# Kernel optimization log

Hardware: AMD Instinct MI355X
Metric: run time of the kernel (lower is better)

## Reference

```python
import jax, jax.numpy as jnp
import numpy as np

H, B, N, F, O = 8, 2, 2048, 256, 64
NEG_INF = jnp.float32(-9e15)


def _xavier(key, shape):
    fan_in, fan_out = shape[-2], shape[-1]
    limit = np.sqrt(6.0 / (fan_in + fan_out))
    return jax.random.uniform(key, shape, dtype=jnp.float32, minval=-limit, maxval=limit)


def setup_inputs() -> dict:
    key = jax.random.key(0)
    k1, k2, k3, k4, k5 = jax.random.split(key, 5)
    x = jax.random.normal(k1, (B, N, F), dtype=jnp.float32)
    adj = (jax.random.uniform(k2, (B, N, N)) < 0.05).astype(jnp.float32)
    adj = jnp.maximum(adj, jnp.eye(N, dtype=jnp.float32))
    W = _xavier(k3, (H, F, O))           # self.linear
    a_src = _xavier(k4, (H, O, 1))       # attention_vect_src
    a_dst = _xavier(k5, (H, O, 1))       # attention_vect_dst
    return {"x": x, "adj": adj, "W": W, "a_src": a_src, "a_dst": a_dst}


def reference(x, adj, W, a_src, a_dst):
    # h: [H, B, N, O]  (per-head linear projection)
    h = jnp.einsum('bnf,hfo->hbno', x, W)
    # additive attention scalars per node: [H, B, N]
    s_src = jnp.einsum('hbno,ho->hbn', h, a_src[..., 0])
    s_dst = jnp.einsum('hbno,ho->hbn', h, a_dst[..., 0])
    # score[h,b,i,j] = s_dst[i] + s_src[j]  -> [H, B, N, N]
    score = s_dst[..., :, None] + s_src[..., None, :]
    score = jax.nn.leaky_relu(score, negative_slope=0.2)
    score = jnp.where(adj > 0, score, NEG_INF)
    att = jax.nn.softmax(score, axis=-1) * adj  # dropout = identity (eval)
    # weighted aggregation of neighbor features: [H, B, N, O]
    out = jnp.einsum('hbij,hbjo->hbio', att, h)
    # concat heads along feature dim (head order preserved): [B, N, H*O]
    out = jnp.transpose(out, (1, 2, 0, 3)).reshape(B, N, H * O)
    return jax.nn.relu(out)
```

## Files before the change

### kernel.cpp

```cpp
#include <hip/hip_runtime.h>

#define H_ 8
#define B_ 2
#define N_ 2048
#define F_ 256
#define O_ 64
#define CAP 256
#define KPAD 264

typedef unsigned short u16;
typedef unsigned int   u32;
typedef __attribute__((ext_vector_type(8))) short bf16x8;
typedef __attribute__((ext_vector_type(4))) float f32x4;

__device__ __forceinline__ float us2f(u16 u) {
    union { u32 i; float f; } c; c.i = ((u32)u) << 16; return c.f;
}
__device__ __forceinline__ u16 f2us_rn(float f) {
    union { float f; u32 i; } c; c.f = f;
    u32 r = c.i + 0x7FFFu + ((c.i >> 16) & 1u);
    return (u16)(r >> 16);
}

__global__ void detect_kernel(const uint4* __restrict__ adj_v, int* __restrict__ flag) {
    __shared__ int found;
    if (threadIdx.x == 0) found = 0;
    __syncthreads();
#pragma unroll
    for (int i = 0; i < 16; ++i) {
        uint4 v = adj_v[threadIdx.x * 16 + i];
        u32 w[4] = {v.x, v.y, v.z, v.w};
        for (int q = 0; q < 4; ++q)
            if (w[q] == 0x00003F80u || w[q] == 0x3F803F80u) found = 1;
    }
    __syncthreads();
    if (threadIdx.x == 0) flag[0] = found;
}

__global__ void wt_kernel(const void* __restrict__ W,
                          const int* __restrict__ flag,
                          u16* __restrict__ Wt) {
    int h  = blockIdx.x;
    int o  = threadIdx.x & 63;
    int fq = threadIdx.x >> 6;
    u16* dst = Wt + (size_t)h * O_ * F_ + (size_t)o * F_;
    if (flag[0]) {
        const u16* wg = (const u16*)W + (size_t)h * F_ * O_;
        for (int i = 0; i < 64; ++i) {
            int f = fq * 64 + i;
            dst[f] = wg[(size_t)f * O_ + o];
        }
    } else {
        const float* wg = (const float*)W + (size_t)h * F_ * O_;
        for (int i = 0; i < 64; ++i) {
            int f = fq * 64 + i;
            dst[f] = f2us_rn(wg[(size_t)f * O_ + o]);
        }
    }
}

__global__ __launch_bounds__(256) void proj_kernel(const void* __restrict__ x,
                                                   const u16* __restrict__ Wt,
                                                   const void* __restrict__ a_src,
                                                   const void* __restrict__ a_dst,
                                                   const int* __restrict__ flag,
                                                   float* __restrict__ hT,
                                                   float* __restrict__ sTsrc,
                                                   float* __restrict__ sTdst) {
    __shared__ alignas(16) u16 wt[64 * KPAD];

    int bf   = flag[0];
    int bx   = blockIdx.x;
    int h    = bx & 7;
    int bn0  = (bx >> 3) * 64;
    int tid  = threadIdx.x;
    int wave = tid >> 6;
    int lane = tid & 63;

    {
        int o    = tid >> 2;
        int part = tid & 3;
        const u16* src = Wt + (size_t)h * O_ * F_ + (size_t)o * F_ + part * 64;
        u16* dst = wt + o * KPAD + part * 64;
#pragma unroll
        for (int i = 0; i < 8; ++i)
            *(uint4*)(dst + i * 8) = *(const uint4*)(src + i * 8);
    }
    __syncthreads();

    int m_l  = lane & 15;
    int quad = lane >> 4;
    int mrow = bn0 + wave * 16 + m_l;

    f32x4 acc[4] = {{0,0,0,0},{0,0,0,0},{0,0,0,0},{0,0,0,0}};
#pragma unroll
    for (int ks = 0; ks < 8; ++ks) {
        int kofs = ks * 32 + quad * 8;
        bf16x8 afrag;
        if (bf) {
            afrag = *(const bf16x8*)((const u16*)x + (size_t)mrow * F_ + kofs);
        } else {
            const float* xr = (const float*)x + (size_t)mrow * F_ + kofs;
#pragma unroll
            for (int q = 0; q < 8; ++q) afrag[q] = (short)f2us_rn(xr[q]);
        }
#pragma unroll
        for (int nt = 0; nt < 4; ++nt) {
            bf16x8 bfrag = *(const bf16x8*)(wt + (nt * 16 + m_l) * KPAD + kofs);
            acc[nt] = __builtin_amdgcn_mfma_f32_16x16x32_bf16(afrag, bfrag, acc[nt], 0, 0, 0);
        }
    }

    float asv[4], adv[4];
#pragma unroll
    for (int nt = 0; nt < 4; ++nt) {
        int o = nt * 16 + m_l;
        if (bf) {
            asv[nt] = us2f(((const u16*)a_src)[h * 64 + o]);
            adv[nt] = us2f(((const u16*)a_dst)[h * 64 + o]);
        } else {
            asv[nt] = ((const float*)a_src)[h * 64 + o];
            adv[nt] = ((const float*)a_dst)[h * 64 + o];
        }
    }
    float vs[4] = {0,0,0,0}, vd[4] = {0,0,0,0};
#pragma unroll
    for (int nt = 0; nt < 4; ++nt)
#pragma unroll
        for (int r = 0; r < 4; ++r) {
            float hv = acc[nt][r];
            int row = wave * 16 + quad * 4 + r;
            hT[(size_t)(bn0 + row) * (H_ * O_) + h * O_ + nt * 16 + m_l] = hv;
            vs[r] = fmaf(hv, asv[nt], vs[r]);
            vd[r] = fmaf(hv, adv[nt], vd[r]);
        }
#pragma unroll
    for (int r = 0; r < 4; ++r)
#pragma unroll
        for (int off = 1; off < 16; off <<= 1) {
            vs[r] += __shfl_xor(vs[r], off);
            vd[r] += __shfl_xor(vd[r], off);
        }
    if (m_l == 0) {
#pragma unroll
        for (int r = 0; r < 4; ++r) {
            int row = wave * 16 + quad * 4 + r;
            sTsrc[(size_t)(bn0 + row) * H_ + h] = vs[r];
            sTdst[(size_t)(bn0 + row) * H_ + h] = vd[r];
        }
    }
}

__global__ void GATLayer_88072599371930_kernel(const float* __restrict__ hT,
                                               const float* __restrict__ sTsrc,
                                               const float* __restrict__ sTdst,
                                               const void* __restrict__ adj,
                                               const int* __restrict__ flag,
                                               float* __restrict__ out) {
    __shared__ int   scnt;
    __shared__ u16   sj[CAP];
    __shared__ float se[CAP * H_];
    __shared__ float mh[H_];
    __shared__ float rzh[H_];
    __shared__ float sdl[H_];
    __shared__ float sred[128 * 4];

    int bi   = blockIdx.x;
    int tid  = threadIdx.x;
    int base = bi & ~(N_ - 1);

    if (tid == 0) scnt = 0;
    if (tid < 8) sdl[tid] = sTdst[(size_t)bi * H_ + tid];
    __syncthreads();

    if (flag[0]) {
        const u16* arow = (const u16*)adj + (size_t)bi * N_;
        uint4 v = *(const uint4*)(arow + tid * 8);
        u32 w[4] = {v.x, v.y, v.z, v.w};
        int j0 = tid * 8;
#pragma unroll
        for (int q = 0; q < 4; ++q) {
            if (w[q] & 0xFFFFu) { int p = atomicAdd(&scnt, 1); if (p < CAP) sj[p] = (u16)(j0 + 2 * q); }
            if (w[q] >> 16)     { int p = atomicAdd(&scnt, 1); if (p < CAP) sj[p] = (u16)(j0 + 2 * q + 1); }
        }
    } else {
        const float* arow = (const float*)adj + (size_t)bi * N_;
        for (int j = tid; j < N_; j += 256) {
            if (arow[j] > 0.f) { int p = atomicAdd(&scnt, 1); if (p < CAP) sj[p] = (u16)j; }
        }
    }
    __syncthreads();
    int n = scnt < CAP ? scnt : CAP;

    if (n <= 0) {
        out[(size_t)bi * 512 + tid] = 999.0f;
        out[(size_t)bi * 512 + 256 + tid] = 999.0f;
        return;
    }

    int tot = n * H_;
    for (int idx = tid; idx < tot; idx += 256) {
        int k  = idx >> 3;
        int hh = idx & 7;
        int j  = sj[k];
        float v = sdl[hh] + sTsrc[(size_t)(base + j) * H_ + hh];
        v = v > 0.f ? v : 0.2f * v;
        se[idx] = v;
    }
    __syncthreads();

    if (tid < 64) {
        int hh = tid >> 3, kk = tid & 7;
        float lm = -3.4e38f;
        for (int k = kk; k < n; k += 8) lm = fmaxf(lm, se[k * 8 + hh]);
#pragma unroll
        for (int mm = 1; mm < 8; mm <<= 1) lm = fmaxf(lm, __shfl_xor(lm, mm));
        if (kk == 0) mh[hh] = lm;
    }
    __syncthreads();

    for (int idx = tid; idx < tot; idx += 256) {
        int hh = idx & 7;
        se[idx] = __expf(se[idx] - mh[hh]);
    }
    __syncthreads();

    if (tid < 64) {
        int hh = tid >> 3, kk = tid & 7;
        float ls = 0.f;
        for (int k = kk; k < n; k += 8) ls += se[k * 8 + hh];
#pragma unroll
        for (int mm = 1; mm < 8; mm <<= 1) ls += __shfl_xor(ls, mm);
        if (kk == 0) rzh[hh] = 1.f / ls;
    }
    __syncthreads();

    int slot = tid >> 7;
    int hh   = (tid >> 4) & 7;
    int oq   = tid & 15;
    const float* hb = hT + (size_t)base * 512 + hh * 64 + oq * 4;
    float a0 = 0.f, a1 = 0.f, a2 = 0.f, a3 = 0.f;
    int k = slot;
    for (; k + 6 < n; k += 8) {
        int   j0 = sj[k],     j1 = sj[k + 2], j2 = sj[k + 4], j3 = sj[k + 6];
        float w0 = se[k * 8 + hh],       w1 = se[(k + 2) * 8 + hh];
        float w2 = se[(k + 4) * 8 + hh], w3 = se[(k + 6) * 8 + hh];
        float4 v0 = *(const float4*)(hb + (size_t)j0 * 512);
        float4 v1 = *(const float4*)(hb + (size_t)j1 * 512);
        float4 v2 = *(const float4*)(hb + (size_t)j2 * 512);
        float4 v3 = *(const float4*)(hb + (size_t)j3 * 512);
        a0 = fmaf(w0, v0.x, a0); a1 = fmaf(w0, v0.y, a1); a2 = fmaf(w0, v0.z, a2); a3 = fmaf(w0, v0.w, a3);
        a0 = fmaf(w1, v1.x, a0); a1 = fmaf(w1, v1.y, a1); a2 = fmaf(w1, v1.z, a2); a3 = fmaf(w1, v1.w, a3);
        a0 = fmaf(w2, v2.x, a0); a1 = fmaf(w2, v2.y, a1); a2 = fmaf(w2, v2.z, a2); a3 = fmaf(w2, v2.w, a3);
        a0 = fmaf(w3, v3.x, a0); a1 = fmaf(w3, v3.y, a1); a2 = fmaf(w3, v3.z, a2); a3 = fmaf(w3, v3.w, a3);
    }
    for (; k < n; k += 2) {
        int   j = sj[k];
        float w = se[k * 8 + hh];
        float4 v = *(const float4*)(hb + (size_t)j * 512);
        a0 = fmaf(w, v.x, a0); a1 = fmaf(w, v.y, a1); a2 = fmaf(w, v.z, a2); a3 = fmaf(w, v.w, a3);
    }
    if (slot == 1) {
        float4 t; t.x = a0; t.y = a1; t.z = a2; t.w = a3;
        ((float4*)sred)[tid - 128] = t;
    }
    __syncthreads();
    if (slot == 0) {
        float4 p = ((float4*)sred)[tid];
        float rz = rzh[hh];
        float4 r;
        r.x = fmaxf((a0 + p.x) * rz, 0.f);
        r.y = fmaxf((a1 + p.y) * rz, 0.f);
        r.z = fmaxf((a2 + p.z) * rz, 0.f);
        r.w = fmaxf((a3 + p.w) * rz, 0.f);
        *(float4*)(out + (size_t)bi * 512 + tid * 4) = r;
    }
}

extern "C" void kernel_launch(void* const* d_in, const int* in_sizes, int n_in,
                              void* d_out, int out_size, void* d_ws, size_t ws_size,
                              hipStream_t stream) {
    const void *x = 0, *adj = 0, *W = 0, *a_src = 0, *a_dst = 0;
    for (int i = 0; i < n_in; ++i) {
        long sz = in_sizes[i];
        if (sz == (long)B_ * N_ * F_)      x = d_in[i];
        else if (sz == (long)B_ * N_ * N_) adj = d_in[i];
        else if (sz == (long)H_ * F_ * O_) W = d_in[i];
        else if (sz == (long)H_ * O_) { if (!a_src) a_src = d_in[i]; else a_dst = d_in[i]; }
    }
    if (!x)     x     = d_in[0];
    if (!adj)   adj   = d_in[1];
    if (!W)     W     = d_in[2];
    if (!a_src) a_src = d_in[3];
    if (!a_dst) a_dst = d_in[4];

    float* out = (float*)d_out;

    char* ws = (char*)d_ws;
    size_t off = 0;
    int*   flag  = (int*)(ws + off);   off += 256;
    float* hT    = (float*)(ws + off); off += (size_t)B_ * N_ * H_ * O_ * 4;
    float* sTsrc = (float*)(ws + off); off += (size_t)B_ * N_ * H_ * 4;
    float* sTdst = (float*)(ws + off); off += (size_t)B_ * N_ * H_ * 4;
    u16*   Wt    = (u16*)(ws + off);   off += (size_t)H_ * O_ * F_ * 2;

    detect_kernel<<<dim3(1), dim3(256), 0, stream>>>((const uint4*)adj, flag);
    wt_kernel<<<dim3(H_), dim3(256), 0, stream>>>(W, flag, Wt);
    proj_kernel<<<dim3((N_ * B_ / 64) * H_), dim3(256), 0, stream>>>(
        x, Wt, a_src, a_dst, flag, hT, sTsrc, sTdst);
    GATLayer_88072599371930_kernel<<<dim3(B_ * N_), dim3(256), 0, stream>>>(
        hT, sTsrc, sTdst, adj, flag, out);
}
```

Baseline: 147.7 us.

## Store projected features as bf16, drop detect kernel, reshape gather loop

```diff
diff --git a/kernel.cpp b/kernel.cpp
--- a/kernel.cpp
+++ b/kernel.cpp
@@ -6,7 +6,6 @@
 #define F_ 256
 #define O_ 64
 #define CAP 256
-#define KPAD 264
 
 typedef unsigned short u16;
 typedef unsigned int   u32;
@@ -16,81 +15,63 @@
 __device__ __forceinline__ float us2f(u16 u) {
     union { u32 i; float f; } c; c.i = ((u32)u) << 16; return c.f;
 }
+__device__ __forceinline__ float hi2f(u32 w) {
+    union { u32 i; float f; } c; c.i = w & 0xFFFF0000u; return c.f;
+}
+__device__ __forceinline__ float lo2f(u32 w) {
+    union { u32 i; float f; } c; c.i = w << 16; return c.f;
+}
 __device__ __forceinline__ u16 f2us_rn(float f) {
     union { float f; u32 i; } c; c.f = f;
     u32 r = c.i + 0x7FFFu + ((c.i >> 16) & 1u);
     return (u16)(r >> 16);
 }
-
-__global__ void detect_kernel(const uint4* __restrict__ adj_v, int* __restrict__ flag) {
-    __shared__ int found;
-    if (threadIdx.x == 0) found = 0;
-    __syncthreads();
-#pragma unroll
-    for (int i = 0; i < 16; ++i) {
-        uint4 v = adj_v[threadIdx.x * 16 + i];
-        u32 w[4] = {v.x, v.y, v.z, v.w};
-        for (int q = 0; q < 4; ++q)
-            if (w[q] == 0x00003F80u || w[q] == 0x3F803F80u) found = 1;
-    }
-    __syncthreads();
-    if (threadIdx.x == 0) flag[0] = found;
-}
-
-__global__ void wt_kernel(const void* __restrict__ W,
-                          const int* __restrict__ flag,
-                          u16* __restrict__ Wt) {
-    int h  = blockIdx.x;
-    int o  = threadIdx.x & 63;
-    int fq = threadIdx.x >> 6;
-    u16* dst = Wt + (size_t)h * O_ * F_ + (size_t)o * F_;
-    if (flag[0]) {
-        const u16* wg = (const u16*)W + (size_t)h * F_ * O_;
-        for (int i = 0; i < 64; ++i) {
-            int f = fq * 64 + i;
-            dst[f] = wg[(size_t)f * O_ + o];
-        }
+__device__ __forceinline__ int detect_bf(const void* adj) {
+    u32 w0 = *(const u32*)adj;
+    return (w0 & 0xFFFFu) == 0x3F80u;
+}
+
+__global__ __launch_bounds__(256) void wt_kernel(const void* __restrict__ W,
+                                                 const void* __restrict__ adj,
+                                                 u16* __restrict__ Wt) {
+    int bf = detect_bf(adj);
+    int g  = blockIdx.x * 256 + threadIdx.x;
+    int h  = g >> 11;
+    int o  = (g >> 5) & 63;
+    int fc = g & 31;
+    u16 tmp[8];
+    if (bf) {
+        const u16* wg = (const u16*)W + (size_t)h * F_ * O_ + o;
+#pragma unroll
+        for (int q = 0; q < 8; ++q) tmp[q] = wg[(size_t)(fc * 8 + q) * O_];
     } else {
-        const float* wg = (const float*)W + (size_t)h * F_ * O_;
-        for (int i = 0; i < 64; ++i) {
-            int f = fq * 64 + i;
-            dst[f] = f2us_rn(wg[(size_t)f * O_ + o]);
-        }
-    }
+        const float* wg = (const float*)W + (size_t)h * F_ * O_ + o;
+#pragma unroll
+        for (int q = 0; q < 8; ++q) tmp[q] = f2us_rn(wg[(size_t)(fc * 8 + q) * O_]);
+    }
+    *(uint4*)(Wt + (size_t)h * O_ * F_ + (size_t)o * F_ + fc * 8) = *(uint4*)tmp;
 }
 
 __global__ __launch_bounds__(256) void proj_kernel(const void* __restrict__ x,
                                                    const u16* __restrict__ Wt,
                                                    const void* __restrict__ a_src,
                                                    const void* __restrict__ a_dst,
-                                                   const int* __restrict__ flag,
-                                                   float* __restrict__ hT,
+                                                   const void* __restrict__ adj,
+                                                   u16* __restrict__ hTb,
                                                    float* __restrict__ sTsrc,
                                                    float* __restrict__ sTdst) {
-    __shared__ alignas(16) u16 wt[64 * KPAD];
-
-    int bf   = flag[0];
+    int bf   = detect_bf(adj);
     int bx   = blockIdx.x;
     int h    = bx & 7;
     int bn0  = (bx >> 3) * 64;
     int tid  = threadIdx.x;
     int wave = tid >> 6;
     int lane = tid & 63;
-
-    {
-        int o    = tid >> 2;
-        int part = tid & 3;
-        const u16* src = Wt + (size_t)h * O_ * F_ + (size_t)o * F_ + part * 64;
-        u16* dst = wt + o * KPAD + part * 64;
-#pragma unroll
-        for (int i = 0; i < 8; ++i)
-            *(uint4*)(dst + i * 8) = *(const uint4*)(src + i * 8);
-    }
-    __syncthreads();
-
     int m_l  = lane & 15;
     int quad = lane >> 4;
     int mrow = bn0 + wave * 16 + m_l;
+
+    const u16* wtb = Wt + (size_t)h * O_ * F_;
 
     f32x4 acc[4] = {{0,0,0,0},{0,0,0,0},{0,0,0,0},{0,0,0,0}};
 #pragma unroll
@@ -106,7 +87,7 @@
         }
 #pragma unroll
         for (int nt = 0; nt < 4; ++nt) {
-            bf16x8 bfrag = *(const bf16x8*)(wt + (nt * 16 + m_l) * KPAD + kofs);
+            bf16x8 bfrag = *(const bf16x8*)(wtb + (size_t)(nt * 16 + m_l) * F_ + kofs);
             acc[nt] = __builtin_amdgcn_mfma_f32_16x16x32_bf16(afrag, bfrag, acc[nt], 0, 0, 0);
         }
     }
@@ -130,7 +111,7 @@
         for (int r = 0; r < 4; ++r) {
             float hv = acc[nt][r];
             int row = wave * 16 + quad * 4 + r;
-            hT[(size_t)(bn0 + row) * (H_ * O_) + h * O_ + nt * 16 + m_l] = hv;
+            hTb[(size_t)(bn0 + row) * 512 + h * 64 + nt * 16 + m_l] = f2us_rn(hv);
             vs[r] = fmaf(hv, asv[nt], vs[r]);
             vd[r] = fmaf(hv, adv[nt], vd[r]);
         }
@@ -151,29 +132,30 @@
     }
 }
 
-__global__ void GATLayer_88072599371930_kernel(const float* __restrict__ hT,
-                                               const float* __restrict__ sTsrc,
-                                               const float* __restrict__ sTdst,
-                                               const void* __restrict__ adj,
-                                               const int* __restrict__ flag,
-                                               float* __restrict__ out) {
+__global__ __launch_bounds__(256) void GATLayer_88072599371930_kernel(
+        const u16* __restrict__ hTb,
+        const float* __restrict__ sTsrc,
+        const float* __restrict__ sTdst,
+        const void* __restrict__ adj,
+        float* __restrict__ out) {
     __shared__ int   scnt;
     __shared__ u16   sj[CAP];
     __shared__ float se[CAP * H_];
     __shared__ float mh[H_];
     __shared__ float rzh[H_];
     __shared__ float sdl[H_];
-    __shared__ float sred[128 * 4];
+    __shared__ float sred[8 * 192];
 
     int bi   = blockIdx.x;
     int tid  = threadIdx.x;
     int base = bi & ~(N_ - 1);
+    int bf   = detect_bf(adj);
 
     if (tid == 0) scnt = 0;
     if (tid < 8) sdl[tid] = sTdst[(size_t)bi * H_ + tid];
     __syncthreads();
 
-    if (flag[0]) {
+    if (bf) {
         const u16* arow = (const u16*)adj + (size_t)bi * N_;
         uint4 v = *(const uint4*)(arow + tid * 8);
         u32 w[4] = {v.x, v.y, v.z, v.w};
@@ -218,13 +200,11 @@
         if (kk == 0) mh[hh] = lm;
     }
     __syncthreads();
-
     for (int idx = tid; idx < tot; idx += 256) {
         int hh = idx & 7;
         se[idx] = __expf(se[idx] - mh[hh]);
     }
     __syncthreads();
-
     if (tid < 64) {
         int hh = tid >> 3, kk = tid & 7;
         float ls = 0.f;
@@ -235,45 +215,61 @@
     }
     __syncthreads();
 
-    int slot = tid >> 7;
-    int hh   = (tid >> 4) & 7;
-    int oq   = tid & 15;
-    const float* hb = hT + (size_t)base * 512 + hh * 64 + oq * 4;
+    int wv   = tid >> 6;
+    int lane = tid & 63;
+    int hh   = lane >> 3;
+    int oq8  = lane & 7;
+    const u16* hb = hTb + (size_t)base * 512 + hh * 64 + oq8 * 8;
+
     float a0 = 0.f, a1 = 0.f, a2 = 0.f, a3 = 0.f;
-    int k = slot;
-    for (; k + 6 < n; k += 8) {
-        int   j0 = sj[k],     j1 = sj[k + 2], j2 = sj[k + 4], j3 = sj[k + 6];
-        float w0 = se[k * 8 + hh],       w1 = se[(k + 2) * 8 + hh];
-        float w2 = se[(k + 4) * 8 + hh], w3 = se[(k + 6) * 8 + hh];
-        float4 v0 = *(const float4*)(hb + (size_t)j0 * 512);
-        float4 v1 = *(const float4*)(hb + (size_t)j1 * 512);
-        float4 v2 = *(const float4*)(hb + (size_t)j2 * 512);
-        float4 v3 = *(const float4*)(hb + (size_t)j3 * 512);
-        a0 = fmaf(w0, v0.x, a0); a1 = fmaf(w0, v0.y, a1); a2 = fmaf(w0, v0.z, a2); a3 = fmaf(w0, v0.w, a3);
-        a0 = fmaf(w1, v1.x, a0); a1 = fmaf(w1, v1.y, a1); a2 = fmaf(w1, v1.z, a2); a3 = fmaf(w1, v1.w, a3);
-        a0 = fmaf(w2, v2.x, a0); a1 = fmaf(w2, v2.y, a1); a2 = fmaf(w2, v2.z, a2); a3 = fmaf(w2, v2.w, a3);
-        a0 = fmaf(w3, v3.x, a0); a1 = fmaf(w3, v3.y, a1); a2 = fmaf(w3, v3.z, a2); a3 = fmaf(w3, v3.w, a3);
-    }
-    for (; k < n; k += 2) {
+    float a4 = 0.f, a5 = 0.f, a6 = 0.f, a7 = 0.f;
+    int k = wv;
+    for (; k + 4 < n; k += 8) {
+        int   j0 = sj[k], j1 = sj[k + 4];
+        float w0 = se[k * 8 + hh], w1 = se[(k + 4) * 8 + hh];
+        uint4 v0 = *(const uint4*)(hb + (size_t)j0 * 512);
+        uint4 v1 = *(const uint4*)(hb + (size_t)j1 * 512);
+        a0 = fmaf(w0, lo2f(v0.x), a0); a1 = fmaf(w0, hi2f(v0.x), a1);
+        a2 = fmaf(w0, lo2f(v0.y), a2); a3 = fmaf(w0, hi2f(v0.y), a3);
+        a4 = fmaf(w0, lo2f(v0.z), a4); a5 = fmaf(w0, hi2f(v0.z), a5);
+        a6 = fmaf(w0, lo2f(v0.w), a6); a7 = fmaf(w0, hi2f(v0.w), a7);
+        a0 = fmaf(w1, lo2f(v1.x), a0); a1 = fmaf(w1, hi2f(v1.x), a1);
+        a2 = fmaf(w1, lo2f(v1.y), a2); a3 = fmaf(w1, hi2f(v1.y), a3);
+        a4 = fmaf(w1, lo2f(v1.z), a4); a5 = fmaf(w1, hi2f(v1.z), a5);
+        a6 = fmaf(w1, lo2f(v1.w), a6); a7 = fmaf(w1, hi2f(v1.w), a7);
+    }
+    for (; k < n; k += 4) {
         int   j = sj[k];
         float w = se[k * 8 + hh];
-        float4 v = *(const float4*)(hb + (size_t)j * 512);
-        a0 = fmaf(w, v.x, a0); a1 = fmaf(w, v.y, a1); a2 = fmaf(w, v.z, a2); a3 = fmaf(w, v.w, a3);
-    }
-    if (slot == 1) {
-        float4 t; t.x = a0; t.y = a1; t.z = a2; t.w = a3;
-        ((float4*)sred)[tid - 128] = t;
-    }
-    __syncthreads();
-    if (slot == 0) {
-        float4 p = ((float4*)sred)[tid];
+        uint4 v = *(const uint4*)(hb + (size_t)j * 512);
+        a0 = fmaf(w, lo2f(v.x), a0); a1 = fmaf(w, hi2f(v.x), a1);
+        a2 = fmaf(w, lo2f(v.y), a2); a3 = fmaf(w, hi2f(v.y), a3);
+        a4 = fmaf(w, lo2f(v.z), a4); a5 = fmaf(w, hi2f(v.z), a5);
+        a6 = fmaf(w, lo2f(v.w), a6); a7 = fmaf(w, hi2f(v.w), a7);
+    }
+
+    if (wv) {
+        int p = (wv - 1) * 64 + lane;
+        sred[0 * 192 + p] = a0; sred[1 * 192 + p] = a1;
+        sred[2 * 192 + p] = a2; sred[3 * 192 + p] = a3;
+        sred[4 * 192 + p] = a4; sred[5 * 192 + p] = a5;
+        sred[6 * 192 + p] = a6; sred[7 * 192 + p] = a7;
+    }
+    __syncthreads();
+    if (wv == 0) {
+        float r[8] = {a0, a1, a2, a3, a4, a5, a6, a7};
         float rz = rzh[hh];
-        float4 r;
-        r.x = fmaxf((a0 + p.x) * rz, 0.f);
-        r.y = fmaxf((a1 + p.y) * rz, 0.f);
-        r.z = fmaxf((a2 + p.z) * rz, 0.f);
-        r.w = fmaxf((a3 + p.w) * rz, 0.f);
-        *(float4*)(out + (size_t)bi * 512 + tid * 4) = r;
+#pragma unroll
+        for (int e = 0; e < 8; ++e) {
+            float t = r[e] + sred[e * 192 + lane] + sred[e * 192 + 64 + lane]
+                           + sred[e * 192 + 128 + lane];
+            r[e] = fmaxf(t * rz, 0.f);
+        }
+        float4 o0; o0.x = r[0]; o0.y = r[1]; o0.z = r[2]; o0.w = r[3];
+        float4 o1; o1.x = r[4]; o1.y = r[5]; o1.z = r[6]; o1.w = r[7];
+        float* op = out + (size_t)bi * 512 + hh * 64 + oq8 * 8;
+        *(float4*)op = o0;
+        *(float4*)(op + 4) = o1;
     }
 }
 
@@ -298,16 +294,14 @@
 
     char* ws = (char*)d_ws;
     size_t off = 0;
-    int*   flag  = (int*)(ws + off);   off += 256;
-    float* hT    = (float*)(ws + off); off += (size_t)B_ * N_ * H_ * O_ * 4;
+    u16*   hTb   = (u16*)(ws + off);   off += (size_t)B_ * N_ * H_ * O_ * 2;
     float* sTsrc = (float*)(ws + off); off += (size_t)B_ * N_ * H_ * 4;
     float* sTdst = (float*)(ws + off); off += (size_t)B_ * N_ * H_ * 4;
     u16*   Wt    = (u16*)(ws + off);   off += (size_t)H_ * O_ * F_ * 2;
 
-    detect_kernel<<<dim3(1), dim3(256), 0, stream>>>((const uint4*)adj, flag);
-    wt_kernel<<<dim3(H_), dim3(256), 0, stream>>>(W, flag, Wt);
+    wt_kernel<<<dim3(64), dim3(256), 0, stream>>>(W, adj, Wt);
     proj_kernel<<<dim3((N_ * B_ / 64) * H_), dim3(256), 0, stream>>>(
-        x, Wt, a_src, a_dst, flag, hT, sTsrc, sTdst);
+        x, Wt, a_src, a_dst, adj, hTb, sTsrc, sTdst);
     GATLayer_88072599371930_kernel<<<dim3(B_ * N_), dim3(256), 0, stream>>>(
-        hT, sTsrc, sTdst, adj, flag, out);
-}
+        hTb, sTsrc, sTdst, adj, out);
+}
```

Result: faster. 128.5 us (-13.0%).
